# Kernel tuning notes

Measured on AMD Instinct MI355X. Metric: run time of the kernel, lower is better.

## Reference

```python
import jax, jax.numpy as jnp
import numpy as np

DICE_W = 0.5
CHAMFER_W = 0.5
SMOOTH = 1e-6


def setup_inputs() -> dict:
    key = jax.random.key(0)
    k1, k2, k3, k4 = jax.random.split(key, 4)
    B, H, W = 4, 1024, 1024
    N = M = 8192
    predictions = jax.random.normal(k1, (B, 1, H, W), dtype=jnp.float32)   # logits
    target = jax.random.uniform(k2, (B, 1, H, W), dtype=jnp.float32)       # soft GT mask
    pred_points = jax.random.normal(k3, (1, N, 2), dtype=jnp.float32)      # pred boundary pts
    target_points = jax.random.normal(k4, (1, M, 2), dtype=jnp.float32)    # GT boundary pts
    return {"predictions": predictions, "target": target,
            "pred_points": pred_points, "target_points": target_points}


def _dice_loss(pred_logits, target):
    pred = jax.nn.sigmoid(pred_logits)
    intersection = jnp.sum(pred * target)
    union = jnp.sum(pred) + jnp.sum(target)
    dice = (2.0 * intersection + SMOOTH) / (union + SMOOTH)
    return 1.0 - dice


def _chamfer_loss(pred_points, target_points):
    # pairwise squared distances: (1, N, M)
    diff = pred_points[:, :, None, :] - target_points[:, None, :, :]
    d2 = jnp.sum(diff * diff, axis=-1)
    # bidirectional chamfer: mean of nearest-neighbor sq-dist in each direction
    return jnp.mean(jnp.min(d2, axis=2)) + jnp.mean(jnp.min(d2, axis=1))


def reference(predictions, target, pred_points, target_points):
    dice = _dice_loss(predictions, target)
    chamfer = _chamfer_loss(pred_points, target_points)
    return DICE_W * dice + CHAMFER_W * chamfer
```

## Files before the change

### kernel.cpp

```cpp
#include <hip/hip_runtime.h>
#include <math.h>

#define INFBITS 0x7F800000u
#define TCH 128
#define PTS 16
#define DICE_BLOCKS 512

__device__ __forceinline__ float block_sum256(float v) {
#pragma unroll
    for (int o = 32; o > 0; o >>= 1) v += __shfl_down(v, o, 64);
    __shared__ float sb[4];
    if ((threadIdx.x & 63) == 0) sb[threadIdx.x >> 6] = v;
    __syncthreads();
    float r = sb[0] + sb[1] + sb[2] + sb[3];
    __syncthreads();
    return r;
}

__global__ void __launch_bounds__(256) fused_partials(
        const float4* __restrict__ p4, const float4* __restrict__ t4, int n4,
        float* __restrict__ inter_p, float* __restrict__ uni_p,
        const float2* __restrict__ P, const float2* __restrict__ T,
        int N, int M, float* __restrict__ pm, int npm, int chm, int gxp,
        unsigned int* __restrict__ counter) {
    int bid = blockIdx.x;
    if (bid == 0 && threadIdx.x == 0) *counter = 0u;

    if (bid < DICE_BLOCKS) {
        float inter = 0.f, uni = 0.f;
#pragma unroll 2
        for (int i = bid * 256 + threadIdx.x; i < n4; i += DICE_BLOCKS * 256) {
            float4 p = p4[i];
            float4 t = t4[i];
            float s;
            s = __fdividef(1.f, 1.f + __expf(-p.x)); inter = fmaf(s, t.x, inter); uni += s + t.x;
            s = __fdividef(1.f, 1.f + __expf(-p.y)); inter = fmaf(s, t.y, inter); uni += s + t.y;
            s = __fdividef(1.f, 1.f + __expf(-p.z)); inter = fmaf(s, t.z, inter); uni += s + t.z;
            s = __fdividef(1.f, 1.f + __expf(-p.w)); inter = fmaf(s, t.w, inter); uni += s + t.w;
        }
        float bi = block_sum256(inter);
        float bu = block_sum256(uni);
        if (threadIdx.x == 0) { inter_p[bid] = bi; uni_p[bid] = bu; }
        return;
    }

    int cb      = bid - DICE_BLOCKS;
    int per_dir = gxp * chm;
    int dir     = cb / per_dir;
    int rem     = cb - dir * per_dir;
    int cy      = rem / gxp;
    int cx      = rem - cy * gxp;
    const float2* A = dir ? T : P;
    const float2* B = dir ? P : T;
    int nA = dir ? M : N;
    int nB = dir ? N : M;

    int tb = cy * TCH;
    if (tb >= nB) return;

    __shared__ float4 bs[TCH];
    int t = threadIdx.x;
    if (t < TCH) {
        float bx = 0.f, by = 0.f, s2 = __uint_as_float(INFBITS);
        if (tb + t < nB) {
            float2 b = B[tb + t];
            bx = b.x; by = b.y;
            s2 = fmaf(bx, bx, by * by);
        }
        bs[t] = make_float4(bx, by, s2, 0.f);
    }
    __syncthreads();

    int abase = cx * (PTS * 256);
    float nx[PTS], ny[PTS], mn[PTS];
#pragma unroll
    for (int i = 0; i < PTS; ++i) {
        int p = abase + i * 256 + t;
        nx[i] = 0.f; ny[i] = 0.f;
        mn[i] = __uint_as_float(INFBITS);
        if (p < nA) {
            float2 a = A[p];
            nx[i] = -2.f * a.x;
            ny[i] = -2.f * a.y;
        }
    }

#pragma unroll 4
    for (int j = 0; j < TCH; ++j) {
        float4 b = bs[j];
#pragma unroll
        for (int i = 0; i < PTS; ++i)
            mn[i] = fminf(mn[i], fmaf(nx[i], b.x, fmaf(ny[i], b.y, b.z)));
    }

    float* dstc = pm + ((size_t)dir * chm + cy) * npm;
#pragma unroll
    for (int i = 0; i < PTS; ++i) {
        int p = abase + i * 256 + t;
        if (p < nA) dstc[p] = mn[i];
    }
}

__global__ void __launch_bounds__(256) finalize_all(
        const float* __restrict__ pm, int npm, int chm,
        int N, int M, int nch0, int nch1,
        const float2* __restrict__ P, const float2* __restrict__ T,
        const float* __restrict__ inter_p, const float* __restrict__ uni_p,
        float* __restrict__ bsum, unsigned int* __restrict__ counter,
        int gxf, float* __restrict__ out) {
    int blk = blockIdx.x;
    int dir = blk / gxf;
    int bx  = blk - dir * gxf;
    int nA  = dir ? M : N;
    int nch = dir ? nch1 : nch0;
    const float2* A = dir ? T : P;

    int p = bx * 256 + threadIdx.x;
    float v = 0.f;
    if (p < nA) {
        const float* src = pm + (size_t)dir * chm * npm + p;
        float m = __uint_as_float(INFBITS);
#pragma unroll 16
        for (int c = 0; c < nch; ++c) m = fminf(m, src[(size_t)c * npm]);
        float2 a = A[p];
        v = m + fmaf(a.x, a.x, a.y * a.y);
    }
    float s = block_sum256(v);

    __shared__ int is_last;
    if (threadIdx.x == 0) {
        bsum[blk] = s;
        __threadfence();
        unsigned int old = atomicAdd(counter, 1u);
        is_last = (old == (unsigned)(2 * gxf - 1));
    }
    __syncthreads();
    if (!is_last) return;
    __threadfence();

    float inter = 0.f, uni = 0.f, c0 = 0.f, c1 = 0.f;
    for (int i = threadIdx.x; i < DICE_BLOCKS; i += 256) {
        inter += inter_p[i];
        uni   += uni_p[i];
    }
    const volatile float* vb = bsum;
    for (int i = threadIdx.x; i < gxf; i += 256) {
        c0 += vb[i];
        c1 += vb[gxf + i];
    }
    float bi  = block_sum256(inter);
    float bu  = block_sum256(uni);
    float bc0 = block_sum256(c0);
    float bc1 = block_sum256(c1);
    if (threadIdx.x == 0) {
        const float SMOOTH = 1e-6f;
        float dice    = (2.f * bi + SMOOTH) / (bu + SMOOTH);
        float chamfer = bc0 / (float)N + bc1 / (float)M;
        out[0] = 0.5f * (1.f - dice) + 0.5f * chamfer;
    }
}

extern "C" void kernel_launch(void* const* d_in, const int* in_sizes, int n_in,
                              void* d_out, int out_size, void* d_ws, size_t ws_size,
                              hipStream_t stream) {
    const float*  pred = (const float*)d_in[0];
    const float*  targ = (const float*)d_in[1];
    const float2* pp   = (const float2*)d_in[2];
    const float2* tp   = (const float2*)d_in[3];
    int n = in_sizes[0];
    int N = in_sizes[2] / 2;
    int M = in_sizes[3] / 2;
    float* out = (float*)d_out;

    int npm  = N > M ? N : M;
    int nch0 = (M + TCH - 1) / TCH;
    int nch1 = (N + TCH - 1) / TCH;
    int chm  = nch0 > nch1 ? nch0 : nch1;
    int gxp  = (npm + PTS * 256 - 1) / (PTS * 256);
    int gxf  = (npm + 255) / 256;

    char*  ws      = (char*)d_ws;
    float* pm      = (float*)ws;
    size_t pm_bytes = (size_t)2 * chm * npm * sizeof(float);
    size_t off     = (pm_bytes + 255) & ~(size_t)255;
    float* inter_p = (float*)(ws + off);
    float* uni_p   = inter_p + DICE_BLOCKS;
    float* bsum    = uni_p + DICE_BLOCKS;
    unsigned int* counter = (unsigned int*)(bsum + 2 * gxf);

    int cham_blocks = 2 * gxp * chm;
    fused_partials<<<DICE_BLOCKS + cham_blocks, 256, 0, stream>>>(
        (const float4*)pred, (const float4*)targ, n / 4,
        inter_p, uni_p, pp, tp, N, M, pm, npm, chm, gxp, counter);

    finalize_all<<<2 * gxf, 256, 0, stream>>>(pm, npm, chm, N, M, nch0, nch1,
                                              pp, tp, inter_p, uni_p, bsum,
                                              counter, gxf, out);
}
```

Baseline: 33.67 us.

## Use packed fp32 FMA over pairs of target points in chamfer inner loop

The chamfer inner loop now processes two B points at once with two-wide float vectors, so the compiler can emit packed FMA instructions (v_pk_fma_f32). Shared memory holds interleaved x/y pairs, and each point's squared norm is recomputed per pair instead of being precomputed. PTS is halved from 16 to 8, which doubles the number of chamfer blocks and lowers register pressure. Padding uses 1e18 instead of infinity, which could matter for very large coordinates, and the float4 load of B assumes 16-byte alignment.

```diff
diff --git a/kernel.cpp b/kernel.cpp
--- a/kernel.cpp
+++ b/kernel.cpp
@@ -3,8 +3,10 @@
 
 #define INFBITS 0x7F800000u
 #define TCH 128
-#define PTS 16
+#define PTS 8
 #define DICE_BLOCKS 512
+
+typedef float v2f __attribute__((ext_vector_type(2)));
 
 __device__ __forceinline__ float block_sum256(float v) {
 #pragma unroll
@@ -58,39 +60,50 @@
     int tb = cy * TCH;
     if (tb >= nB) return;
 
-    __shared__ float4 bs[TCH];
+    __shared__ __align__(16) float4 qs[TCH / 2];
     int t = threadIdx.x;
-    if (t < TCH) {
-        float bx = 0.f, by = 0.f, s2 = __uint_as_float(INFBITS);
-        if (tb + t < nB) {
-            float2 b = B[tb + t];
-            bx = b.x; by = b.y;
-            s2 = fmaf(bx, bx, by * by);
-        }
-        bs[t] = make_float4(bx, by, s2, 0.f);
+    if (t < TCH / 2) {
+        int j0 = tb + 2 * t;
+        float4 r = make_float4(1e18f, 1e18f, 1e18f, 1e18f);
+        if (j0 + 1 < nB) {
+            float4 b = *(const float4*)&B[j0];
+            r = make_float4(b.x, b.z, b.y, b.w);
+        } else if (j0 < nB) {
+            float2 b = B[j0];
+            r = make_float4(b.x, 1e18f, b.y, 1e18f);
+        }
+        qs[t] = r;
     }
     __syncthreads();
 
     int abase = cx * (PTS * 256);
-    float nx[PTS], ny[PTS], mn[PTS];
+    v2f nx2[PTS], ny2[PTS];
+    float mn[PTS];
 #pragma unroll
     for (int i = 0; i < PTS; ++i) {
         int p = abase + i * 256 + t;
-        nx[i] = 0.f; ny[i] = 0.f;
+        float nx = 0.f, ny = 0.f;
         mn[i] = __uint_as_float(INFBITS);
         if (p < nA) {
             float2 a = A[p];
-            nx[i] = -2.f * a.x;
-            ny[i] = -2.f * a.y;
-        }
+            nx = -2.f * a.x;
+            ny = -2.f * a.y;
+        }
+        nx2[i] = (v2f){nx, nx};
+        ny2[i] = (v2f){ny, ny};
     }
 
 #pragma unroll 4
-    for (int j = 0; j < TCH; ++j) {
-        float4 b = bs[j];
-#pragma unroll
-        for (int i = 0; i < PTS; ++i)
-            mn[i] = fminf(mn[i], fmaf(nx[i], b.x, fmaf(ny[i], b.y, b.z)));
+    for (int jp = 0; jp < TCH / 2; ++jp) {
+        float4 q = qs[jp];
+        v2f X = (v2f){q.x, q.y};
+        v2f Y = (v2f){q.z, q.w};
+        v2f S = X * X + Y * Y;
+#pragma unroll
+        for (int i = 0; i < PTS; ++i) {
+            v2f D = nx2[i] * X + (ny2[i] * Y + S);
+            mn[i] = fminf(fminf(mn[i], D.x), D.y);
+        }
     }
 
     float* dstc = pm + ((size_t)dir * chm + cy) * npm;
```

After: 28.38 us, median of 2. -15.7%, faster.
